# Kernel tuning notes

Measured on AMD Instinct MI355X. Metric: run time of the kernel, lower is better.

The kernel has to match this reference:

```python
import jax, jax.numpy as jnp
import numpy as np

T, B, D, H = 1024, 8, 1024, 16
HD = D // H  # head_dim = 64


def setup_inputs() -> dict:
    key = jax.random.key(0)
    ks = jax.random.split(key, 11)
    s = 1.0 / np.sqrt(D)
    return {
        "query": jax.random.normal(ks[0], (T, B, D), jnp.float32),
        "key": jax.random.normal(ks[1], (T, B, D), jnp.float32),
        "value": jax.random.normal(ks[2], (T, B, D), jnp.float32),
        "Wq": jax.random.normal(ks[3], (D, D), jnp.float32) * s,
        "bq": jax.random.normal(ks[4], (D,), jnp.float32) * s,
        "Wk": jax.random.normal(ks[5], (D, D), jnp.float32) * s,
        "bk": jax.random.normal(ks[6], (D,), jnp.float32) * s,
        "Wv": jax.random.normal(ks[7], (D, D), jnp.float32) * s,
        "bv": jax.random.normal(ks[8], (D,), jnp.float32) * s,
        "Wo": jax.random.normal(ks[9], (D, D), jnp.float32) * s,
        "bo": jax.random.normal(ks[10], (D,), jnp.float32) * s,
    }


def reference(query, key, value, Wq, bq, Wk, bk, Wv, bv, Wo, bo):
    # query/key/value: (T, B, D) seq-first, as in nn.MultiheadAttention
    t, b, d = query.shape
    scale = HD ** -0.5
    # projections (torch Linear: x @ W.T + b), split into heads -> (B, H, T, HD)
    q = (query @ Wq.T + bq).reshape(t, b, H, HD).transpose(1, 2, 0, 3)
    k = (key @ Wk.T + bk).reshape(t, b, H, HD).transpose(1, 2, 0, 3)
    v = (value @ Wv.T + bv).reshape(t, b, H, HD).transpose(1, 2, 0, 3)
    # full (B, H, T, T) scores, matching the module's explicit materialization
    attn = jnp.einsum('bhtd,bhsd->bhts', q, k) * scale
    attn = jax.nn.softmax(attn, axis=-1)
    # (B, H, T, HD) -> (T, B, D)
    out = jnp.einsum('bhts,bhsd->bhtd', attn, v)
    out = out.transpose(2, 0, 1, 3).reshape(t, b, d)
    return out @ Wo.T + bo
```

## Files before the change

### kernel.cpp

```cpp
#include <hip/hip_runtime.h>

#define T_SEQ 1024
#define BATCH 8
#define DMODEL 1024
#define NHEAD 16
#define HDIM 64
#define M_ROWS (T_SEQ * BATCH)
#define QSCALE (0.125f * 1.44269504088896f)

typedef unsigned short ushort_t;
typedef __attribute__((ext_vector_type(8))) short short8;
typedef __attribute__((ext_vector_type(4))) float f32x4;

#define G2L16(g, l) __builtin_amdgcn_global_load_lds(                      \
    (const __attribute__((address_space(1))) void*)(g),                    \
    (__attribute__((address_space(3))) void*)(l), 16, 0, 0)

#define SBAR()  __builtin_amdgcn_s_barrier()
#define LGKM0() asm volatile("s_waitcnt lgkmcnt(0)" ::: "memory")

static __device__ __forceinline__ ushort_t f2bf(float f) {
    unsigned int u = __builtin_bit_cast(unsigned int, f);
    u += 0x7FFFu + ((u >> 16) & 1u);
    return (ushort_t)(u >> 16);
}

#if __has_builtin(__builtin_amdgcn_cvt_pk_bf16_f32)
typedef __attribute__((ext_vector_type(2))) __bf16 bf16x2_t;
static __device__ __forceinline__ unsigned pk2(float lo, float hi) {
    bf16x2_t r = __builtin_amdgcn_cvt_pk_bf16_f32(lo, hi);
    return __builtin_bit_cast(unsigned, r);
}
#else
static __device__ __forceinline__ unsigned pk2(float lo, float hi) {
    return (unsigned)f2bf(lo) | ((unsigned)f2bf(hi) << 16);
}
#endif

#if __has_builtin(__builtin_amdgcn_exp2f)
#define EXP2F(x) __builtin_amdgcn_exp2f(x)
#else
#define EXP2F(x) exp2f(x)
#endif

__global__ __launch_bounds__(256) void cast_all_bf16(
    const float4* __restrict__ s0, const float4* __restrict__ s1,
    const float4* __restrict__ s2, const float4* __restrict__ s3,
    const float4* __restrict__ s4, const float4* __restrict__ s5,
    const float4* __restrict__ s6,
    uint2* __restrict__ d0, uint2* __restrict__ d1, uint2* __restrict__ d2,
    uint2* __restrict__ d3, uint2* __restrict__ d4, uint2* __restrict__ d5,
    uint2* __restrict__ d6, int n4big, int n4small)
{
    const int y = blockIdx.y;
    const int n4 = (y < 3) ? n4big : n4small;
    const int i = blockIdx.x * 256 + threadIdx.x;
    if (i >= n4) return;
    const float4* s; uint2* d;
    switch (y) {
        case 0: s = s0; d = d0; break;
        case 1: s = s1; d = d1; break;
        case 2: s = s2; d = d2; break;
        case 3: s = s3; d = d3; break;
        case 4: s = s4; d = d4; break;
        case 5: s = s5; d = d5; break;
        default: s = s6; d = d6; break;
    }
    float4 v = s[i];
    uint2 o; o.x = pk2(v.x, v.y); o.y = pk2(v.z, v.w);
    d[i] = o;
}

template<bool OUT_BF16>
__global__ __launch_bounds__(512) void gemm256_bt(
    const ushort_t* __restrict__ A, const ushort_t* __restrict__ Wbase,
    const float* __restrict__ bias0, const float* __restrict__ bias1,
    const float* __restrict__ bias2, void* __restrict__ Yv,
    int N, int K, float scale0)
{
    __shared__ ushort_t As[2][256 * 64];
    __shared__ ushort_t Bs[2][256 * 64];

    const int tid  = threadIdx.x;
    const int lane = tid & 63;
    const int w    = tid >> 6;
    const int wm   = w >> 2;
    const int wn   = w & 3;
    const int quad = lane >> 4;
    const int l16  = lane & 15;
    const int srow = lane >> 3;
    const int sch  = lane & 7;

    const int nwg = gridDim.x * gridDim.y;
    const int lin = blockIdx.y * gridDim.x + blockIdx.x;
    const int qq  = nwg >> 3;
    const int swz = (lin & 7) * qq + (lin >> 3);
    const int bn  = swz & 3;
    const int bmg = swz >> 2;

    const int sel = bmg >> 5;
    const ushort_t* Wb = Wbase + (size_t)sel * N * K;
    const float* bias = (sel == 0) ? bias0 : (sel == 1) ? bias1 : bias2;
    const float scale = (sel == 0) ? scale0 : 1.0f;

    const size_t arow0 = (size_t)bmg * 256;
    const size_t brow0 = (size_t)bn * 256;
    const int scol = (sch ^ srow) * 8;

    size_t aoff[2][2], boff[2][2];
#pragma unroll
    for (int h = 0; h < 2; h++)
#pragma unroll
        for (int u = 0; u < 2; u++) {
            const int rl = h * 128 + (w * 2 + u) * 8 + srow;
            aoff[h][u] = (arow0 + rl) * (size_t)K + scol;
            boff[h][u] = (brow0 + rl) * (size_t)K + scol;
        }

    const int c0 = (quad ^ (l16 & 7)) * 8;
    const int c1 = c0 ^ 32;

    const f32x4 zero4 = {0.f, 0.f, 0.f, 0.f};
    f32x4 acc[8][4];
#pragma unroll
    for (int i = 0; i < 8; i++)
#pragma unroll
        for (int j = 0; j < 4; j++) acc[i][j] = zero4;

    short8 a0[4][2], a1[4][2];
    short8 b0[2][2], b1[2][2];

    const int nT = K >> 6;

#define STAGE_A(t, buf, h)                                                  \
    do {                                                                    \
        G2L16(A + aoff[h][0] + (t) * 64,                                    \
              (char*)&As[buf][0] + (h) * 16384 + (w * 2 + 0) * 1024);       \
        G2L16(A + aoff[h][1] + (t) * 64,                                    \
              (char*)&As[buf][0] + (h) * 16384 + (w * 2 + 1) * 1024);       \
    } while (0)
#define STAGE_B(t, buf, h)                                                  \
    do {                                                                    \
        G2L16(Wb + boff[h][0] + (t) * 64,                                   \
              (char*)&Bs[buf][0] + (h) * 16384 + (w * 2 + 0) * 1024);       \
        G2L16(Wb + boff[h][1] + (t) * 64,                                   \
              (char*)&Bs[buf][0] + (h) * 16384 + (w * 2 + 1) * 1024);       \
    } while (0)

    STAGE_A(0, 0, 0); STAGE_A(0, 0, 1);
    STAGE_B(0, 0, 0); STAGE_B(0, 0, 1);
    STAGE_B(1, 1, 0); STAGE_B(1, 1, 1);
    asm volatile("s_waitcnt vmcnt(4)" ::: "memory");
    SBAR();

    for (int kt = 0; kt < nT; ++kt) {
        const int cur = kt & 1;

#pragma unroll
        for (int ii = 0; ii < 4; ii++) {
            const int row = wm * 128 + ii * 16 + l16;
            a0[ii][0] = *(const short8*)&As[cur][row * 64 + c0];
            a0[ii][1] = *(const short8*)&As[cur][row * 64 + c1];
        }
#pragma unroll
        for (int jj = 0; jj < 2; jj++) {
            const int row = wn * 64 + jj * 16 + l16;
            b0[jj][0] = *(const short8*)&Bs[cur][row * 64 + c0];
            b0[jj][1] = *(const short8*)&Bs[cur][row * 64 + c1];
        }
        if (kt + 1 < nT) STAGE_A(kt + 1, cur ^ 1, 0);
        SBAR();
        LGKM0();
        __builtin_amdgcn_s_setprio(1);
#pragma unroll
        for (int ii = 0; ii < 4; ii++)
#pragma unroll
            for (int jj = 0; jj < 2; jj++)
#pragma unroll
                for (int ks = 0; ks < 2; ks++)
                    acc[ii][jj] = __builtin_amdgcn_mfma_f32_16x16x32_bf16(
                        a0[ii][ks], b0[jj][ks], acc[ii][jj], 0, 0, 0);
        __builtin_amdgcn_s_setprio(0);
        SBAR();

#pragma unroll
        for (int jj = 0; jj < 2; jj++) {
            const int row = wn * 64 + 32 + jj * 16 + l16;
            b1[jj][0] = *(const short8*)&Bs[cur][row * 64 + c0];
            b1[jj][1] = *(const short8*)&Bs[cur][row * 64 + c1];
        }
        if (kt + 1 < nT) STAGE_A(kt + 1, cur ^ 1, 1);
        SBAR();
        LGKM0();
        __builtin_amdgcn_s_setprio(1);
#pragma unroll
        for (int ii = 0; ii < 4; ii++)
#pragma unroll
            for (int jj = 0; jj < 2; jj++)
#pragma unroll
                for (int ks = 0; ks < 2; ks++)
                    acc[ii][2 + jj] = __builtin_amdgcn_mfma_f32_16x16x32_bf16(
                        a0[ii][ks], b1[jj][ks], acc[ii][2 + jj], 0, 0, 0);
        __builtin_amdgcn_s_setprio(0);
        SBAR();

#pragma unroll
        for (int ii = 0; ii < 4; ii++) {
            const int row = wm * 128 + 64 + ii * 16 + l16;
            a1[ii][0] = *(const short8*)&As[cur][row * 64 + c0];
            a1[ii][1] = *(const short8*)&As[cur][row * 64 + c1];
        }
        if (kt + 2 < nT) STAGE_B(kt + 2, cur, 0);
        SBAR();
        LGKM0();
        __builtin_amdgcn_s_setprio(1);
#pragma unroll
        for (int ii = 0; ii < 4; ii++)
#pragma unroll
            for (int jj = 0; jj < 2; jj++)
#pragma unroll
                for (int ks = 0; ks < 2; ks++)
                    acc[4 + ii][jj] = __builtin_amdgcn_mfma_f32_16x16x32_bf16(
                        a1[ii][ks], b0[jj][ks], acc[4 + ii][jj], 0, 0, 0);
        __builtin_amdgcn_s_setprio(0);
        SBAR();

        if (kt + 2 < nT) STAGE_B(kt + 2, cur, 1);
        SBAR();
        __builtin_amdgcn_s_setprio(1);
#pragma unroll
        for (int ii = 0; ii < 4; ii++)
#pragma unroll
            for (int jj = 0; jj < 2; jj++)
#pragma unroll
                for (int ks = 0; ks < 2; ks++)
                    acc[4 + ii][2 + jj] = __builtin_amdgcn_mfma_f32_16x16x32_bf16(
                        a1[ii][ks], b1[jj][ks], acc[4 + ii][2 + jj], 0, 0, 0);
        __builtin_amdgcn_s_setprio(0);
        if (kt < nT - 2) asm volatile("s_waitcnt vmcnt(4)" ::: "memory");
        else             asm volatile("s_waitcnt vmcnt(0)" ::: "memory");
        SBAR();
    }
#undef STAGE_A
#undef STAGE_B

    float bj[4];
#pragma unroll
    for (int j = 0; j < 4; j++) bj[j] = bias[bn * 256 + wn * 64 + j * 16 + l16];
#pragma unroll
    for (int il = 0; il < 8; il++) {
#pragma unroll
        for (int r = 0; r < 4; r++) {
            const size_t row = (size_t)bmg * 256 + wm * 128 + il * 16 + quad * 4 + r;
#pragma unroll
            for (int j = 0; j < 4; j++) {
                const int col = bn * 256 + wn * 64 + j * 16 + l16;
                const float v = (acc[il][j][r] + bj[j]) * scale;
                if (OUT_BF16) ((ushort_t*)Yv)[row * N + col] = f2bf(v);
                else          ((float*)   Yv)[row * N + col] = v;
            }
        }
    }
}

template<bool OUT_BF16>
__global__ __launch_bounds__(256) void gemm_bt_mfma(
    const ushort_t* __restrict__ A, const ushort_t* __restrict__ Wbase,
    const float* __restrict__ bias0, const float* __restrict__ bias1,
    const float* __restrict__ bias2, void* __restrict__ Yv,
    int N, int K, float scale0)
{
    __shared__ ushort_t As[128 * 64];
    __shared__ ushort_t Bs[128 * 64];

    const int tid  = threadIdx.x;
    const int lane = tid & 63;
    const int quad = lane >> 4;
    const int l16  = lane & 15;
    const int w    = tid >> 6;
    const int wm   = w >> 1;
    const int wn   = w & 1;
    const int bn   = blockIdx.x;
    const int bmg  = blockIdx.y;

    const int sel = bmg >> 6;
    const ushort_t* Wb = Wbase + (size_t)sel * N * K;
    const float* bias = (sel == 0) ? bias0 : (sel == 1) ? bias1 : bias2;
    const float scale = (sel == 0) ? scale0 : 1.0f;

    const int srow_in = lane >> 3;
    const int sch     = lane & 7;

    const f32x4 zero4 = {0.f, 0.f, 0.f, 0.f};
    f32x4 acc[4][4];
#pragma unroll
    for (int i = 0; i < 4; i++)
#pragma unroll
        for (int j = 0; j < 4; j++) acc[i][j] = zero4;

    for (int k0 = 0; k0 < K; k0 += 64) {
        __syncthreads();
#pragma unroll
        for (int u = 0; u < 4; u++) {
            int seg = w * 4 + u;
            int row = seg * 8 + srow_in;
            int chs = sch ^ (row & 7);
            G2L16(&A [(size_t)(bmg * 128 + row) * K + k0 + chs * 8],
                  (char*)As + seg * 1024);
            G2L16(&Wb[(size_t)(bn  * 128 + row) * K + k0 + chs * 8],
                  (char*)Bs + seg * 1024);
        }
        __syncthreads();

#pragma unroll
        for (int ks = 0; ks < 2; ks++) {
            short8 af[4], bfr[4];
#pragma unroll
            for (int i = 0; i < 4; i++) {
                int row = wm * 64 + i * 16 + l16;
                af[i] = *(const short8*)&As[row * 64 + (((ks * 4 + quad) ^ (row & 7)) * 8)];
            }
#pragma unroll
            for (int j = 0; j < 4; j++) {
                int row = wn * 64 + j * 16 + l16;
                bfr[j] = *(const short8*)&Bs[row * 64 + (((ks * 4 + quad) ^ (row & 7)) * 8)];
            }
#pragma unroll
            for (int i = 0; i < 4; i++)
#pragma unroll
                for (int j = 0; j < 4; j++)
                    acc[i][j] = __builtin_amdgcn_mfma_f32_16x16x32_bf16(
                        af[i], bfr[j], acc[i][j], 0, 0, 0);
        }
    }

    float bj[4];
#pragma unroll
    for (int j = 0; j < 4; j++) bj[j] = bias[bn * 128 + wn * 64 + j * 16 + l16];
#pragma unroll
    for (int i = 0; i < 4; i++) {
#pragma unroll
        for (int r = 0; r < 4; r++) {
            size_t row = (size_t)(bmg * 128 + wm * 64 + i * 16 + quad * 4 + r);
#pragma unroll
            for (int j = 0; j < 4; j++) {
                int col = bn * 128 + wn * 64 + j * 16 + l16;
                float v = (acc[i][j][r] + bj[j]) * scale;
                if (OUT_BF16) ((ushort_t*)Yv)[row * N + col] = f2bf(v);
                else          ((float*)   Yv)[row * N + col] = v;
            }
        }
    }
}

__global__ __launch_bounds__(256) void transpose_v(
    const ushort_t* __restrict__ Vp, ushort_t* __restrict__ Vt)
{
    __shared__ ushort_t Ts[64][72];
    const int tid = threadIdx.x;
    const int t0 = blockIdx.x * 64;
    const int bh = blockIdx.y;
    const int b = bh >> 4, h = bh & 15;

#pragma unroll
    for (int u = 0; u < 2; u++) {
        int e = u * 256 + tid;
        int row = e >> 3, ch = (e & 7) * 8;
        uint4 v = *(const uint4*)&Vp[((size_t)(t0 + row) * BATCH + b) * DMODEL + h * 64 + ch];
        *(uint4*)&Ts[row][ch] = v;
    }
    __syncthreads();
#pragma unroll
    for (int u = 0; u < 2; u++) {
        int e = u * 256 + tid;
        int d = e >> 3, tc = (e & 7) * 8;
        uint4 o;
        o.x = (unsigned)Ts[tc + 0][d] | ((unsigned)Ts[tc + 1][d] << 16);
        o.y = (unsigned)Ts[tc + 2][d] | ((unsigned)Ts[tc + 3][d] << 16);
        o.z = (unsigned)Ts[tc + 4][d] | ((unsigned)Ts[tc + 5][d] << 16);
        o.w = (unsigned)Ts[tc + 6][d] | ((unsigned)Ts[tc + 7][d] << 16);
        *(uint4*)&Vt[((size_t)(bh * 64 + d)) * T_SEQ + t0 + tc] = o;
    }
}

__global__ __launch_bounds__(256) void attn_mfma(
    const ushort_t* __restrict__ Qp, const ushort_t* __restrict__ Kp,
    const ushort_t* __restrict__ VtG, ushort_t* __restrict__ Ao)
{
    __shared__ ushort_t Ks[64 * 64];
    __shared__ ushort_t Vs[64 * 64];
    __shared__ ushort_t Pl[4][32][72];

    const int tid  = threadIdx.x;
    const int lane = tid & 63;
    const int w    = tid >> 6;
    const int quad = lane >> 4;
    const int l16  = lane & 15;
    const int bid  = blockIdx.x;
    const int qb   = bid >> 7;
    const int bh   = bid & 127;
    const int b    = bh >> 4, h = bh & 15;
    const int hoff = h * 64;
    const int q0   = qb * 128 + w * 32;

    const int srow_in = lane >> 3;
    const int sch     = lane & 7;

    short8 qf[2][2];
#pragma unroll
    for (int rt = 0; rt < 2; rt++)
#pragma unroll
        for (int ks = 0; ks < 2; ks++)
            qf[rt][ks] = *(const short8*)&Qp[((size_t)(q0 + rt * 16 + l16) * BATCH + b) * DMODEL
                                             + hoff + ks * 32 + quad * 8];

    short8 ones;
#pragma unroll
    for (int i = 0; i < 8; i++) ones[i] = (short)0x3F80;

    const f32x4 zero4 = {0.f, 0.f, 0.f, 0.f};
    f32x4 oacc[2][4], lacc[2];
#pragma unroll
    for (int rt = 0; rt < 2; rt++) {
        lacc[rt] = zero4;
#pragma unroll
        for (int c = 0; c < 4; c++) oacc[rt][c] = zero4;
    }

    for (int s0 = 0; s0 < T_SEQ; s0 += 64) {
        __syncthreads();
#pragma unroll
        for (int u = 0; u < 2; u++) {
            int seg = w * 2 + u;
            int row = seg * 8 + srow_in;
            int chs = sch ^ (row & 7);
            G2L16(&Kp[((size_t)(s0 + row) * BATCH + b) * DMODEL + hoff + chs * 8],
                  (char*)Ks + seg * 1024);
            G2L16(&VtG[((size_t)(bh * 64 + row)) * T_SEQ + s0 + chs * 8],
                  (char*)Vs + seg * 1024);
        }
        __syncthreads();

        f32x4 sacc[2][4];
#pragma unroll
        for (int rt = 0; rt < 2; rt++)
#pragma unroll
            for (int c = 0; c < 4; c++) sacc[rt][c] = zero4;
#pragma unroll
        for (int c = 0; c < 4; c++) {
            int row = c * 16 + l16;
#pragma unroll
            for (int ks = 0; ks < 2; ks++) {
                short8 kf = *(const short8*)&Ks[row * 64 + (((ks * 4 + quad) ^ (row & 7)) * 8)];
#pragma unroll
                for (int rt = 0; rt < 2; rt++)
                    sacc[rt][c] = __builtin_amdgcn_mfma_f32_16x16x32_bf16(
                        kf, qf[rt][ks], sacc[rt][c], 0, 0, 0);
            }
        }

#pragma unroll
        for (int rt = 0; rt < 2; rt++)
#pragma unroll
            for (int c = 0; c < 4; c++) {
                uint2 pv;
                pv.x = pk2(EXP2F(sacc[rt][c][0]), EXP2F(sacc[rt][c][1]));
                pv.y = pk2(EXP2F(sacc[rt][c][2]), EXP2F(sacc[rt][c][3]));
                *(uint2*)&Pl[w][rt * 16 + l16][c * 16 + quad * 4] = pv;
            }

        short8 pf[2][2];
#pragma unroll
        for (int rt = 0; rt < 2; rt++)
#pragma unroll
            for (int ks = 0; ks < 2; ks++)
                pf[rt][ks] = *(const short8*)&Pl[w][rt * 16 + l16][ks * 32 + quad * 8];

#pragma unroll
        for (int rt = 0; rt < 2; rt++)
#pragma unroll
            for (int ks = 0; ks < 2; ks++)
                lacc[rt] = __builtin_amdgcn_mfma_f32_16x16x32_bf16(
                    ones, pf[rt][ks], lacc[rt], 0, 0, 0);

#pragma unroll
        for (int dt = 0; dt < 4; dt++) {
            int row = dt * 16 + l16;
#pragma unroll
            for (int ks = 0; ks < 2; ks++) {
                short8 vf = *(const short8*)&Vs[row * 64 + (((ks * 4 + quad) ^ (row & 7)) * 8)];
#pragma unroll
                for (int rt = 0; rt < 2; rt++)
                    oacc[rt][dt] = __builtin_amdgcn_mfma_f32_16x16x32_bf16(
                        vf, pf[rt][ks], oacc[rt][dt], 0, 0, 0);
            }
        }
    }

#pragma unroll
    for (int rt = 0; rt < 2; rt++) {
        float inv = 1.f / lacc[rt][0];
#pragma unroll
        for (int dt = 0; dt < 4; dt++) {
            uint2 ov;
            ov.x = pk2(oacc[rt][dt][0] * inv, oacc[rt][dt][1] * inv);
            ov.y = pk2(oacc[rt][dt][2] * inv, oacc[rt][dt][3] * inv);
            *(uint2*)&Pl[w][rt * 16 + l16][dt * 16 + quad * 4] = ov;
        }
    }
#pragma unroll
    for (int it = 0; it < 4; it++) {
        int row = it * 8 + (lane >> 3);
        int ch  = lane & 7;
        uint4 val = *(const uint4*)&Pl[w][row][ch * 8];
        *(uint4*)&Ao[((size_t)(q0 + row) * BATCH + b) * DMODEL + hoff + ch * 8] = val;
    }
}

extern "C" void kernel_launch(void* const* d_in, const int* in_sizes, int n_in,
                              void* d_out, int out_size, void* d_ws, size_t ws_size,
                              hipStream_t stream)
{
    const float* q  = (const float*)d_in[0];
    const float* k  = (const float*)d_in[1];
    const float* v  = (const float*)d_in[2];
    const float* Wq = (const float*)d_in[3];
    const float* bq = (const float*)d_in[4];
    const float* Wk = (const float*)d_in[5];
    const float* bk = (const float*)d_in[6];
    const float* Wv = (const float*)d_in[7];
    const float* bv = (const float*)d_in[8];
    const float* Wo = (const float*)d_in[9];
    const float* bo = (const float*)d_in[10];

    ushort_t* ws = (ushort_t*)d_ws;
    const size_t E = (size_t)M_ROWS * DMODEL;
    const size_t EW = (size_t)DMODEL * DMODEL;
    ushort_t* qb  = ws;
    ushort_t* kb  = ws + E;
    ushort_t* vb  = ws + 2 * E;
    ushort_t* Qp  = ws + 3 * E;
    ushort_t* Kp  = ws + 4 * E;
    ushort_t* Vp  = ws + 5 * E;
    ushort_t* Wqb = ws + 6 * E;
    ushort_t* Wkb = Wqb + EW;
    ushort_t* Wvb = Wkb + EW;
    ushort_t* Wob = Wvb + EW;
    ushort_t* Vt  = qb;
    ushort_t* Aob = kb;

    const int n4_in = (int)(E / 4);
    const int n4_w  = (int)(EW / 4);
    cast_all_bf16<<<dim3(n4_in / 256, 7), 256, 0, stream>>>(
        (const float4*)q, (const float4*)k, (const float4*)v,
        (const float4*)Wq, (const float4*)Wk, (const float4*)Wv, (const float4*)Wo,
        (uint2*)qb, (uint2*)kb, (uint2*)vb,
        (uint2*)Wqb, (uint2*)Wkb, (uint2*)Wvb, (uint2*)Wob,
        n4_in, n4_w);

    gemm256_bt<true><<<dim3(DMODEL / 256, 3 * M_ROWS / 256), 512, 0, stream>>>(
        qb, Wqb, bq, bk, bv, Qp, DMODEL, DMODEL, QSCALE);

    transpose_v<<<dim3(T_SEQ / 64, BATCH * NHEAD), 256, 0, stream>>>(Vp, Vt);

    attn_mfma<<<dim3(8 * 128), 256, 0, stream>>>(Qp, Kp, Vt, Aob);

    gemm_bt_mfma<false><<<dim3(DMODEL / 128, M_ROWS / 128), 256, 0, stream>>>(
        Aob, Wob, bo, bo, bo, d_out, DMODEL, DMODEL, 1.0f);
}
```

Before: 319.2 us.

## Restructure GEMM barrier schedule and double-buffer K/V tiles in attention

The projection GEMM main loop goes from four barriers per k-step to two, with whole A and B tile prefetches issued in two batches behind sched_barrier fences. The attention kernel gains double-buffered K/V shared tiles, so the next tile's global-to-LDS load overlaps the current tile's MFMAs, and the MFMA blocks are wrapped in setprio. This targets barrier stalls and exposed load latency. It doubles K/V LDS use, which may lower occupancy, and the reordered waits must still keep buffer reuse safe.

```diff
diff --git a/kernel.cpp b/kernel.cpp
--- a/kernel.cpp
+++ b/kernel.cpp
@@ -16,8 +16,9 @@
     (const __attribute__((address_space(1))) void*)(g),                    \
     (__attribute__((address_space(3))) void*)(l), 16, 0, 0)
 
-#define SBAR()  __builtin_amdgcn_s_barrier()
-#define LGKM0() asm volatile("s_waitcnt lgkmcnt(0)" ::: "memory")
+#define SBAR()   __builtin_amdgcn_s_barrier()
+#define LGKM0()  asm volatile("s_waitcnt lgkmcnt(0)" ::: "memory")
+#define SCHEDB() __builtin_amdgcn_sched_barrier(0)
 
 static __device__ __forceinline__ ushort_t f2bf(float f) {
     unsigned int u = __builtin_bit_cast(unsigned int, f);
@@ -127,9 +128,6 @@
 #pragma unroll
         for (int j = 0; j < 4; j++) acc[i][j] = zero4;
 
-    short8 a0[4][2], a1[4][2];
-    short8 b0[2][2], b1[2][2];
-
     const int nT = K >> 6;
 
 #define STAGE_A(t, buf, h)                                                  \
@@ -150,12 +148,17 @@
     STAGE_A(0, 0, 0); STAGE_A(0, 0, 1);
     STAGE_B(0, 0, 0); STAGE_B(0, 0, 1);
     STAGE_B(1, 1, 0); STAGE_B(1, 1, 1);
-    asm volatile("s_waitcnt vmcnt(4)" ::: "memory");
-    SBAR();
 
     for (int kt = 0; kt < nT; ++kt) {
         const int cur = kt & 1;
 
+        if (kt < nT - 1) asm volatile("s_waitcnt vmcnt(4)" ::: "memory");
+        else             asm volatile("s_waitcnt vmcnt(0)" ::: "memory");
+        SBAR();
+        SCHEDB();
+        if (kt + 1 < nT) { STAGE_A(kt + 1, cur ^ 1, 0); STAGE_A(kt + 1, cur ^ 1, 1); }
+
+        short8 a0[4][2], b0[2][2], b1[2][2];
 #pragma unroll
         for (int ii = 0; ii < 4; ii++) {
             const int row = wm * 128 + ii * 16 + l16;
@@ -168,9 +171,6 @@
             b0[jj][0] = *(const short8*)&Bs[cur][row * 64 + c0];
             b0[jj][1] = *(const short8*)&Bs[cur][row * 64 + c1];
         }
-        if (kt + 1 < nT) STAGE_A(kt + 1, cur ^ 1, 0);
-        SBAR();
-        LGKM0();
         __builtin_amdgcn_s_setprio(1);
 #pragma unroll
         for (int ii = 0; ii < 4; ii++)
@@ -181,17 +181,12 @@
                     acc[ii][jj] = __builtin_amdgcn_mfma_f32_16x16x32_bf16(
                         a0[ii][ks], b0[jj][ks], acc[ii][jj], 0, 0, 0);
         __builtin_amdgcn_s_setprio(0);
-        SBAR();
-
 #pragma unroll
         for (int jj = 0; jj < 2; jj++) {
             const int row = wn * 64 + 32 + jj * 16 + l16;
             b1[jj][0] = *(const short8*)&Bs[cur][row * 64 + c0];
             b1[jj][1] = *(const short8*)&Bs[cur][row * 64 + c1];
         }
-        if (kt + 1 < nT) STAGE_A(kt + 1, cur ^ 1, 1);
-        SBAR();
-        LGKM0();
         __builtin_amdgcn_s_setprio(1);
 #pragma unroll
         for (int ii = 0; ii < 4; ii++)
@@ -202,17 +197,19 @@
                     acc[ii][2 + jj] = __builtin_amdgcn_mfma_f32_16x16x32_bf16(
                         a0[ii][ks], b1[jj][ks], acc[ii][2 + jj], 0, 0, 0);
         __builtin_amdgcn_s_setprio(0);
+
+        LGKM0();
         SBAR();
-
+        SCHEDB();
+        if (kt + 2 < nT) { STAGE_B(kt + 2, cur, 0); STAGE_B(kt + 2, cur, 1); }
+
+        short8 a1[4][2];
 #pragma unroll
         for (int ii = 0; ii < 4; ii++) {
             const int row = wm * 128 + 64 + ii * 16 + l16;
             a1[ii][0] = *(const short8*)&As[cur][row * 64 + c0];
             a1[ii][1] = *(const short8*)&As[cur][row * 64 + c1];
         }
-        if (kt + 2 < nT) STAGE_B(kt + 2, cur, 0);
-        SBAR();
-        LGKM0();
         __builtin_amdgcn_s_setprio(1);
 #pragma unroll
         for (int ii = 0; ii < 4; ii++)
@@ -222,12 +219,6 @@
                 for (int ks = 0; ks < 2; ks++)
                     acc[4 + ii][jj] = __builtin_amdgcn_mfma_f32_16x16x32_bf16(
                         a1[ii][ks], b0[jj][ks], acc[4 + ii][jj], 0, 0, 0);
-        __builtin_amdgcn_s_setprio(0);
-        SBAR();
-
-        if (kt + 2 < nT) STAGE_B(kt + 2, cur, 1);
-        SBAR();
-        __builtin_amdgcn_s_setprio(1);
 #pragma unroll
         for (int ii = 0; ii < 4; ii++)
 #pragma unroll
@@ -237,9 +228,6 @@
                     acc[4 + ii][2 + jj] = __builtin_amdgcn_mfma_f32_16x16x32_bf16(
                         a1[ii][ks], b1[jj][ks], acc[4 + ii][2 + jj], 0, 0, 0);
         __builtin_amdgcn_s_setprio(0);
-        if (kt < nT - 2) asm volatile("s_waitcnt vmcnt(4)" ::: "memory");
-        else             asm volatile("s_waitcnt vmcnt(0)" ::: "memory");
-        SBAR();
     }
 #undef STAGE_A
 #undef STAGE_B
@@ -387,8 +375,8 @@
     const ushort_t* __restrict__ Qp, const ushort_t* __restrict__ Kp,
     const ushort_t* __restrict__ VtG, ushort_t* __restrict__ Ao)
 {
-    __shared__ ushort_t Ks[64 * 64];
-    __shared__ ushort_t Vs[64 * 64];
+    __shared__ ushort_t Ks[2][64 * 64];
+    __shared__ ushort_t Vs[2][64 * 64];
     __shared__ ushort_t Pl[4][32][72];
 
     const int tid  = threadIdx.x;
@@ -427,37 +415,49 @@
         for (int c = 0; c < 4; c++) oacc[rt][c] = zero4;
     }
 
-    for (int s0 = 0; s0 < T_SEQ; s0 += 64) {
-        __syncthreads();
-#pragma unroll
-        for (int u = 0; u < 2; u++) {
-            int seg = w * 2 + u;
-            int row = seg * 8 + srow_in;
-            int chs = sch ^ (row & 7);
-            G2L16(&Kp[((size_t)(s0 + row) * BATCH + b) * DMODEL + hoff + chs * 8],
-                  (char*)Ks + seg * 1024);
-            G2L16(&VtG[((size_t)(bh * 64 + row)) * T_SEQ + s0 + chs * 8],
-                  (char*)Vs + seg * 1024);
-        }
-        __syncthreads();
+#define STAGE_KV(s0_, buf)                                                       \
+    do {                                                                         \
+        _Pragma("unroll")                                                        \
+        for (int u = 0; u < 2; u++) {                                            \
+            int seg = w * 2 + u;                                                 \
+            int row = seg * 8 + srow_in;                                         \
+            int chs = sch ^ (row & 7);                                           \
+            G2L16(&Kp[((size_t)((s0_) + row) * BATCH + b) * DMODEL + hoff + chs * 8], \
+                  (char*)&Ks[buf][0] + seg * 1024);                              \
+            G2L16(&VtG[((size_t)(bh * 64 + row)) * T_SEQ + (s0_) + chs * 8],     \
+                  (char*)&Vs[buf][0] + seg * 1024);                              \
+        }                                                                        \
+    } while (0)
+
+    STAGE_KV(0, 0);
+
+    for (int it = 0; it < 16; ++it) {
+        const int cur = it & 1;
+
+        asm volatile("s_waitcnt vmcnt(0)" ::: "memory");
+        SBAR();
+        SCHEDB();
+        if (it + 1 < 16) STAGE_KV((it + 1) * 64, cur ^ 1);
 
         f32x4 sacc[2][4];
 #pragma unroll
         for (int rt = 0; rt < 2; rt++)
 #pragma unroll
             for (int c = 0; c < 4; c++) sacc[rt][c] = zero4;
+        __builtin_amdgcn_s_setprio(1);
 #pragma unroll
         for (int c = 0; c < 4; c++) {
             int row = c * 16 + l16;
 #pragma unroll
             for (int ks = 0; ks < 2; ks++) {
-                short8 kf = *(const short8*)&Ks[row * 64 + (((ks * 4 + quad) ^ (row & 7)) * 8)];
+                short8 kf = *(const short8*)&Ks[cur][row * 64 + (((ks * 4 + quad) ^ (row & 7)) * 8)];
 #pragma unroll
                 for (int rt = 0; rt < 2; rt++)
                     sacc[rt][c] = __builtin_amdgcn_mfma_f32_16x16x32_bf16(
                         kf, qf[rt][ks], sacc[rt][c], 0, 0, 0);
             }
         }
+        __builtin_amdgcn_s_setprio(0);
 
 #pragma unroll
         for (int rt = 0; rt < 2; rt++)
@@ -483,19 +483,24 @@
                 lacc[rt] = __builtin_amdgcn_mfma_f32_16x16x32_bf16(
                     ones, pf[rt][ks], lacc[rt], 0, 0, 0);
 
+        __builtin_amdgcn_s_setprio(1);
 #pragma unroll
         for (int dt = 0; dt < 4; dt++) {
             int row = dt * 16 + l16;
 #pragma unroll
             for (int ks = 0; ks < 2; ks++) {
-                short8 vf = *(const short8*)&Vs[row * 64 + (((ks * 4 + quad) ^ (row & 7)) * 8)];
+                short8 vf = *(const short8*)&Vs[cur][row * 64 + (((ks * 4 + quad) ^ (row & 7)) * 8)];
 #pragma unroll
                 for (int rt = 0; rt < 2; rt++)
                     oacc[rt][dt] = __builtin_amdgcn_mfma_f32_16x16x32_bf16(
                         vf, pf[rt][ks], oacc[rt][dt], 0, 0, 0);
             }
         }
-    }
+        __builtin_amdgcn_s_setprio(0);
+
+        LGKM0();
+    }
+#undef STAGE_KV
 
 #pragma unroll
     for (int rt = 0; rt < 2; rt++) {
```

Result: no change. 323.2 us (+1.2%).
